# Performance work log

Hardware: AMD Instinct MI355X
Metric: run time of the kernel (lower is better)

## Reference

```python
import jax, jax.numpy as jnp
import numpy as np


def _gcn_conv(x, src, dst, W, b, n):
    # PyG GCNConv: linear -> add self-loops -> symmetric degree norm -> scatter-add -> bias
    h = x @ W  # [N, out]
    e = src.shape[0]
    loop = jnp.arange(n, dtype=src.dtype)
    s = jnp.concatenate([src, loop])
    d = jnp.concatenate([dst, loop])
    w = jnp.ones(e + n, dtype=x.dtype)
    deg = jax.ops.segment_sum(w, d, num_segments=n)              # in-degree incl. self-loop
    dinv = jnp.where(deg > 0, jax.lax.rsqrt(deg), 0.0)
    norm = dinv[s] * dinv[d]                                     # [E+N]
    out = jax.ops.segment_sum(h[s] * norm[:, None], d, num_segments=n)
    return out + b


def setup_inputs() -> dict:
    key = jax.random.key(0)
    ks = jax.random.split(key, 8)
    N, E = 100000, 1600000
    in_dim, hid, hid1, out_dim = 256, 128, 64, 40
    x = jax.random.normal(ks[0], (N, in_dim), dtype=jnp.float32)
    edge_index = jax.random.randint(ks[1], (2, E), 0, N, dtype=jnp.int32)
    W1 = jax.random.normal(ks[2], (in_dim, hid), dtype=jnp.float32) * (1.0 / np.sqrt(in_dim))
    b1 = jnp.zeros((hid,), jnp.float32)
    W2 = jax.random.normal(ks[3], (hid, hid1), dtype=jnp.float32) * (1.0 / np.sqrt(hid))
    b2 = jnp.zeros((hid1,), jnp.float32)
    Wo = jax.random.normal(ks[4], (hid1, out_dim), dtype=jnp.float32) * (1.0 / np.sqrt(hid1))
    bo = jnp.zeros((out_dim,), jnp.float32)
    return {"x": x, "edge_index": edge_index, "W1": W1, "b1": b1,
            "W2": W2, "b2": b2, "Wo": Wo, "bo": bo}


def reference(x, edge_index, W1, b1, W2, b2, Wo, bo):
    n = x.shape[0]
    src, dst = edge_index[0], edge_index[1]
    h = jax.nn.relu(_gcn_conv(x, src, dst, W1, b1, n))
    # F.dropout(training=False) is identity in inference
    h = _gcn_conv(h, src, dst, W2, b2, n)
    logits = h @ Wo + bo
    return jax.nn.log_softmax(logits, axis=1)
```

## Files before the change

### kernel.cpp

```cpp
#include <hip/hip_runtime.h>
#include <hip/hip_bf16.h>

typedef unsigned short u16;
typedef unsigned int u32;
typedef __attribute__((ext_vector_type(8))) short bf16x8;
typedef __attribute__((ext_vector_type(4))) float f32x4;
typedef __attribute__((ext_vector_type(4))) u16 u16x4;

__device__ __forceinline__ u16 f2bf(float f) {
    __hip_bfloat16 h = __float2bfloat16(f);
    return *reinterpret_cast<u16*>(&h);
}
__device__ __forceinline__ float bf_lo(u32 u) {
    union { u32 u; float f; } v; v.u = u << 16; return v.f;
}
__device__ __forceinline__ float bf_hi(u32 u) {
    union { u32 u; float f; } v; v.u = u & 0xFFFF0000u; return v.f;
}
__device__ __forceinline__ u32 pack2(float a, float b) {
    return (u32)f2bf(a) | ((u32)f2bf(b) << 16);
}

#define NB2 256
#define CHUNK 2048

__global__ void init_kernel(const float* __restrict__ W1, u16* __restrict__ B1, int K1, int N1,
                            const float* __restrict__ W2, u16* __restrict__ B2, int K2, int N2,
                            int* __restrict__ bcur, u32* __restrict__ g1pad,
                            u32* __restrict__ g2pad) {
    int i = blockIdx.x * 256 + threadIdx.x;
    int sz1 = K1 * N1;
    if (i < sz1) {
        int n = i / K1, k = i - n * K1;
        B1[i] = f2bf(W1[(size_t)k * N1 + n]);
    } else if (i - sz1 < K2 * N2) {
        int j = i - sz1;
        int n = j / K2, k = j - n * K2;
        B2[j] = f2bf(W2[(size_t)k * N2 + n]);
    }
    if (blockIdx.x == 0) {
        int t = threadIdx.x;
        bcur[t] = 0;
        if (t < 64) g1pad[t] = 0;
        if (t < 32) g2pad[t] = 0;
    }
}

__launch_bounds__(256)
__global__ void route(const int* __restrict__ src, const int* __restrict__ dst, int E, int R2,
                      int* __restrict__ bcur, int2* __restrict__ bp, int bcap) {
    __shared__ int cnt[NB2];
    __shared__ int cur[NB2];
    const int tid = threadIdx.x;
    const int base = blockIdx.x * CHUNK;
    cnt[tid] = 0;
    __syncthreads();
#pragma unroll
    for (int i = 0; i < CHUNK / 256; i++) {
        int e = base + i * 256 + tid;
        if (e < E) atomicAdd(&cnt[dst[e] / R2], 1);
    }
    __syncthreads();
    {
        int c = cnt[tid];
        cur[tid] = c ? atomicAdd(&bcur[tid], c) : 0;
    }
    __syncthreads();
#pragma unroll
    for (int i = 0; i < CHUNK / 256; i++) {
        int e = base + i * 256 + tid;
        if (e < E) {
            int d = dst[e], s = src[e];
            int b = d / R2;
            int pos = atomicAdd(&cur[b], 1);
            if (pos < bcap) bp[(size_t)b * bcap + pos] = (int2){s, d};
        }
    }
}

__launch_bounds__(256)
__global__ void build_csr(const int2* __restrict__ bp2, const int* __restrict__ bcnt2, int bcap2,
                          int sreg, int R2, int N,
                          int* __restrict__ rs, int* __restrict__ re,
                          float* __restrict__ dinv, int* __restrict__ srcids) {
    __shared__ int2 pl[8300];
    __shared__ int bins[400];
    __shared__ int tsum[256];
    const int b = blockIdx.x;
    const int tid = threadIdx.x;
    const int lo = b * R2;
    int hi = lo + R2; if (hi > N) hi = N;
    const int nb = hi - lo;
    if (nb <= 0) return;
    int cnt = bcnt2[b];
    if (cnt > bcap2) cnt = bcap2;
    const int2* mine = bp2 + (size_t)b * bcap2;

    for (int i = tid; i < nb; i += 256) bins[i] = 0;
    for (int i = tid; i < cnt; i += 256) pl[i] = mine[i];
    __syncthreads();
    for (int i = tid; i < cnt; i += 256) atomicAdd(&bins[pl[i].y - lo], 1);
    __syncthreads();

    const int base4 = tid * 4;
    int creal[4], cpad[4], ex[4];
    int run = 0;
#pragma unroll
    for (int k = 0; k < 4; k++) {
        int idx = base4 + k;
        creal[k] = 0; cpad[k] = 0; ex[k] = 0;
        if (idx < nb) {
            int c = bins[idx];
            creal[k] = c;
            cpad[k] = (c + 3) & ~3;
            dinv[lo + idx] = rsqrtf((float)c + 1.0f);
            ex[k] = run;
            run += cpad[k];
        }
    }
    tsum[tid] = run;
    __syncthreads();
    for (int off = 1; off < 256; off <<= 1) {
        int u = (tid >= off) ? tsum[tid - off] : 0;
        __syncthreads();
        tsum[tid] += u;
        __syncthreads();
    }
    const int toff = ((tid > 0) ? tsum[tid - 1] : 0) + b * sreg;
    __syncthreads();
#pragma unroll
    for (int k = 0; k < 4; k++) {
        int idx = base4 + k;
        if (idx < nb) {
            int st = toff + ex[k];
            bins[idx] = st;
            rs[lo + idx] = st;
            re[lo + idx] = st + cpad[k];
            for (int q = creal[k]; q < cpad[k]; q++) srcids[st + q] = N;
        }
    }
    __syncthreads();
    for (int i = tid; i < cnt; i += 256) {
        int2 p = pl[i];
        int pos = atomicAdd(&bins[p.y - lo], 1);
        srcids[pos] = p.x;
    }
}

template <int K, int BN, int IFR, int JFR, int WM, int WN, bool ABF16>
__launch_bounds__(256)
__global__ void gemm_mfma(const void* __restrict__ Av, const u16* __restrict__ Bt,
                          const float* __restrict__ dinv, u16* __restrict__ G, int M) {
    constexpr int BM = 128, BK = 32, BKP = 40;
    __shared__ u16 As[BM][BKP];
    __shared__ u16 Bs[BN][BKP];
    const int tid = threadIdx.x;
    const int lane = tid & 63, wave = tid >> 6;
    const int r = lane & 15, g = lane >> 4;
    const int wm = wave % WM, wn = wave / WM;
    const int m0 = blockIdx.x * BM;

    f32x4 acc[IFR][JFR];
#pragma unroll
    for (int i = 0; i < IFR; i++)
#pragma unroll
        for (int j = 0; j < JFR; j++) acc[i][j] = (f32x4){0.f, 0.f, 0.f, 0.f};

    for (int k0 = 0; k0 < K; k0 += BK) {
#pragma unroll
        for (int p = 0; p < 4; p++) {
            int q = tid + p * 256;
            int row = q >> 3, kq = (q & 7) << 2;
            int gr = m0 + row; if (gr >= M) gr = M - 1;
            if constexpr (ABF16) {
                const u16* A = (const u16*)Av;
                *(u16x4*)&As[row][kq] = *(const u16x4*)(A + (size_t)gr * K + k0 + kq);
            } else {
                const float* A = (const float*)Av;
                float4 a = *(const float4*)(A + (size_t)gr * K + k0 + kq);
                u16x4 v = { f2bf(a.x), f2bf(a.y), f2bf(a.z), f2bf(a.w) };
                *(u16x4*)&As[row][kq] = v;
            }
        }
#pragma unroll
        for (int p = 0; p < BN / 32; p++) {
            int q = tid + p * 256;
            int row = q >> 3, kq = (q & 7) << 2;
            *(u16x4*)&Bs[row][kq] = *(const u16x4*)(Bt + (size_t)row * K + k0 + kq);
        }
        __syncthreads();

        bf16x8 af[IFR], bfr[JFR];
#pragma unroll
        for (int i = 0; i < IFR; i++)
            af[i] = *(const bf16x8*)&As[wm * (IFR * 16) + i * 16 + r][g * 8];
#pragma unroll
        for (int j = 0; j < JFR; j++)
            bfr[j] = *(const bf16x8*)&Bs[wn * (JFR * 16) + j * 16 + r][g * 8];
#pragma unroll
        for (int i = 0; i < IFR; i++)
#pragma unroll
            for (int j = 0; j < JFR; j++)
                acc[i][j] = __builtin_amdgcn_mfma_f32_16x16x32_bf16(af[i], bfr[j], acc[i][j], 0, 0, 0);
        __syncthreads();
    }

#pragma unroll
    for (int i = 0; i < IFR; i++) {
#pragma unroll
        for (int t = 0; t < 4; t++) {
            int row = m0 + wm * (IFR * 16) + i * 16 + g * 4 + t;
            if (row < M) {
                float dn = dinv[row];
#pragma unroll
                for (int j = 0; j < JFR; j++) {
                    int col = wn * (JFR * 16) + j * 16 + r;
                    G[(size_t)row * BN + col] = f2bf(acc[i][j][t] * dn);
                }
            }
        }
    }
}

#define ACC8(v) { a0 += bf_lo(v.x); a1 += bf_hi(v.x); a2 += bf_lo(v.y); a3 += bf_hi(v.y); \
                  a4 += bf_lo(v.z); a5 += bf_hi(v.z); a6 += bf_lo(v.w); a7 += bf_hi(v.w); }

__launch_bounds__(256)
__global__ void agg128(const uint4* __restrict__ g1, const float4* __restrict__ bias,
                       const int* __restrict__ rs, const int* __restrict__ re,
                       const int* __restrict__ srcids, const float* __restrict__ dinv,
                       uint4* __restrict__ h1, int n) {
    const int tq = threadIdx.x >> 4;
    const int c  = threadIdx.x & 15;
    const int node = blockIdx.x * 16 + tq;
    if (node >= n) return;
    const float dn = dinv[node];
    uint4 sv = g1[(size_t)node * 16 + c];
    float a0 = bf_lo(sv.x), a1 = bf_hi(sv.x), a2 = bf_lo(sv.y), a3 = bf_hi(sv.y);
    float a4 = bf_lo(sv.z), a5 = bf_hi(sv.z), a6 = bf_lo(sv.w), a7 = bf_hi(sv.w);

    int j = rs[node] >> 2;
    const int jend = re[node] >> 2;
    const int4* ip = (const int4*)srcids;
    if (j < jend) {
        int4 idx = ip[j];
        for (++j; j < jend; ++j) {
            uint4 v0 = g1[(size_t)idx.x * 16 + c];
            uint4 v1 = g1[(size_t)idx.y * 16 + c];
            uint4 v2 = g1[(size_t)idx.z * 16 + c];
            uint4 v3 = g1[(size_t)idx.w * 16 + c];
            int4 nxt = ip[j];
            ACC8(v0); ACC8(v1); ACC8(v2); ACC8(v3);
            idx = nxt;
        }
        uint4 v0 = g1[(size_t)idx.x * 16 + c];
        uint4 v1 = g1[(size_t)idx.y * 16 + c];
        uint4 v2 = g1[(size_t)idx.z * 16 + c];
        uint4 v3 = g1[(size_t)idx.w * 16 + c];
        ACC8(v0); ACC8(v1); ACC8(v2); ACC8(v3);
    }

    float4 b0 = bias[c * 2], b1v = bias[c * 2 + 1];
    uint4 w;
    w.x = pack2(fmaxf(a0 * dn + b0.x, 0.f), fmaxf(a1 * dn + b0.y, 0.f));
    w.y = pack2(fmaxf(a2 * dn + b0.z, 0.f), fmaxf(a3 * dn + b0.w, 0.f));
    w.z = pack2(fmaxf(a4 * dn + b1v.x, 0.f), fmaxf(a5 * dn + b1v.y, 0.f));
    w.w = pack2(fmaxf(a6 * dn + b1v.z, 0.f), fmaxf(a7 * dn + b1v.w, 0.f));
    h1[(size_t)node * 16 + c] = w;
}

__launch_bounds__(256)
__global__ void agg64out(const uint2* __restrict__ g2, const float4* __restrict__ bias,
                         const int* __restrict__ rs, const int* __restrict__ re,
                         const int* __restrict__ srcids, const float* __restrict__ dinv,
                         const float* __restrict__ Wo, const float* __restrict__ bo,
                         float* __restrict__ out, int n) {
    __shared__ float Ws[64 * 40];
    __shared__ float bs[40];
    __shared__ float h2s[16][68];
    for (int i = threadIdx.x; i < 64 * 40; i += 256) Ws[i] = Wo[i];
    if (threadIdx.x < 40) bs[threadIdx.x] = bo[threadIdx.x];

    const int tq = threadIdx.x >> 4;
    const int c  = threadIdx.x & 15;
    const int node = blockIdx.x * 16 + tq;
    if (node < n) {
        const float dn = dinv[node];
        uint2 sv = g2[(size_t)node * 16 + c];
        float a0 = bf_lo(sv.x), a1 = bf_hi(sv.x), a2 = bf_lo(sv.y), a3 = bf_hi(sv.y);
        int j = rs[node] >> 2;
        const int jend = re[node] >> 2;
        const int4* ip = (const int4*)srcids;
        if (j < jend) {
            int4 idx = ip[j];
            for (++j; j < jend; ++j) {
                uint2 v0 = g2[(size_t)idx.x * 16 + c];
                uint2 v1 = g2[(size_t)idx.y * 16 + c];
                uint2 v2 = g2[(size_t)idx.z * 16 + c];
                uint2 v3 = g2[(size_t)idx.w * 16 + c];
                int4 nxt = ip[j];
                a0 += (bf_lo(v0.x) + bf_lo(v1.x)) + (bf_lo(v2.x) + bf_lo(v3.x));
                a1 += (bf_hi(v0.x) + bf_hi(v1.x)) + (bf_hi(v2.x) + bf_hi(v3.x));
                a2 += (bf_lo(v0.y) + bf_lo(v1.y)) + (bf_lo(v2.y) + bf_lo(v3.y));
                a3 += (bf_hi(v0.y) + bf_hi(v1.y)) + (bf_hi(v2.y) + bf_hi(v3.y));
                idx = nxt;
            }
            uint2 v0 = g2[(size_t)idx.x * 16 + c];
            uint2 v1 = g2[(size_t)idx.y * 16 + c];
            uint2 v2 = g2[(size_t)idx.z * 16 + c];
            uint2 v3 = g2[(size_t)idx.w * 16 + c];
            a0 += (bf_lo(v0.x) + bf_lo(v1.x)) + (bf_lo(v2.x) + bf_lo(v3.x));
            a1 += (bf_hi(v0.x) + bf_hi(v1.x)) + (bf_hi(v2.x) + bf_hi(v3.x));
            a2 += (bf_lo(v0.y) + bf_lo(v1.y)) + (bf_lo(v2.y) + bf_lo(v3.y));
            a3 += (bf_hi(v0.y) + bf_hi(v1.y)) + (bf_hi(v2.y) + bf_hi(v3.y));
        }
        float4 bb = bias[c];
        float4 hv = { a0 * dn + bb.x, a1 * dn + bb.y, a2 * dn + bb.z, a3 * dn + bb.w };
        *(float4*)&h2s[tq][c * 4] = hv;
    }
    __syncthreads();

    if (node < n) {
        const int j2 = (c < 8) ? (c + 32) : 39;
        float l0 = bs[c], l1 = bs[c + 16], l2 = bs[j2];
#pragma unroll 8
        for (int k = 0; k < 64; k++) {
            float hk = h2s[tq][k];
            l0 = fmaf(hk, Ws[k * 40 + c], l0);
            l1 = fmaf(hk, Ws[k * 40 + c + 16], l1);
            l2 = fmaf(hk, Ws[k * 40 + j2], l2);
        }
        float m = fmaxf(fmaxf(l0, l1), (c < 8) ? l2 : -3.0e38f);
#pragma unroll
        for (int o = 1; o < 16; o <<= 1) m = fmaxf(m, __shfl_xor(m, o));
        float s = expf(l0 - m) + expf(l1 - m) + ((c < 8) ? expf(l2 - m) : 0.f);
#pragma unroll
        for (int o = 1; o < 16; o <<= 1) s += __shfl_xor(s, o);
        float lse = m + logf(s);
        float* op = out + (size_t)node * 40;
        op[c] = l0 - lse;
        op[c + 16] = l1 - lse;
        if (c < 8) op[c + 32] = l2 - lse;
    }
}

extern "C" void kernel_launch(void* const* d_in, const int* in_sizes, int n_in,
                              void* d_out, int out_size, void* d_ws, size_t ws_size,
                              hipStream_t stream) {
    const float* x  = (const float*)d_in[0];
    const int*   ei = (const int*)d_in[1];
    const float* W1 = (const float*)d_in[2];
    const float* b1 = (const float*)d_in[3];
    const float* W2 = (const float*)d_in[4];
    const float* b2 = (const float*)d_in[5];
    const float* Wo = (const float*)d_in[6];
    const float* bo = (const float*)d_in[7];
    float* out = (float*)d_out;

    const int HID  = in_sizes[3];
    const int IN   = in_sizes[2] / HID;
    const int HID1 = in_sizes[5];
    const int N = in_sizes[0] / IN;
    const int E = in_sizes[1] / 2;
    const int* src = ei;
    const int* dst = ei + E;

    const int R2 = (N + NB2 - 1) / NB2;
    const int bcap2 = E / NB2 + 2048;
    const int sreg  = (bcap2 + 3 * R2 + 32 + 3) & ~3;

    char* ws = (char*)d_ws;
    size_t off = 0;
    auto alloc = [&](size_t bytes) -> void* {
        void* p = ws + off;
        off += (bytes + 255) / 256 * 256;
        return p;
    };
    float* dinv   = (float*)alloc((size_t)N * 4);
    int*   rs     = (int*)alloc((size_t)N * 4);
    int*   re     = (int*)alloc((size_t)N * 4);
    int*   bcur   = (int*)alloc(NB2 * 4);
    int*   srcids = (int*)alloc((size_t)NB2 * sreg * 4);
    u16*   W1t    = (u16*)alloc((size_t)IN * HID * 2);
    u16*   W2t    = (u16*)alloc((size_t)HID * HID1 * 2);
    size_t bp2Bytes = (size_t)NB2 * bcap2 * 8;
    size_t gBytes = (size_t)(N + 1) * HID * 2;
    size_t sharedBytes = (gBytes > bp2Bytes) ? gBytes : bp2Bytes;
    char*  shared = (char*)alloc(sharedBytes);
    int2*  bp2    = (int2*)shared;
    u16*   g1     = (u16*)shared;
    u16*   h1     = (u16*)alloc((size_t)N * HID * 2);
    u16*   g2     = (u16*)alloc((size_t)(N + 1) * HID1 * 2);

    init_kernel<<<(IN * HID + HID * HID1 + 255) / 256, 256, 0, stream>>>(
        W1, W1t, IN, HID, W2, W2t, HID, HID1,
        bcur, (u32*)g1 + (size_t)N * 64, (u32*)g2 + (size_t)N * 32);

    const int nchunk = (E + CHUNK - 1) / CHUNK;
    route<<<nchunk, 256, 0, stream>>>(src, dst, E, R2, bcur, bp2, bcap2);
    build_csr<<<NB2, 256, 0, stream>>>(bp2, bcur, bcap2, sreg, R2, N, rs, re, dinv, srcids);

    const int gblocks = (N + 127) / 128;
    gemm_mfma<256, 128, 4, 4, 2, 2, false><<<gblocks, 256, 0, stream>>>(x, W1t, dinv, g1, N);
    agg128<<<(N + 15) / 16, 256, 0, stream>>>((const uint4*)g1, (const float4*)b1,
                                              rs, re, srcids, dinv, (uint4*)h1, N);

    gemm_mfma<128, 64, 2, 4, 4, 1, true><<<gblocks, 256, 0, stream>>>(h1, W2t, dinv, g2, N);
    agg64out<<<(N + 15) / 16, 256, 0, stream>>>((const uint2*)g2, (const float4*)b2,
                                                rs, re, srcids, dinv, Wo, bo, out, N);

    (void)ws_size; (void)n_in; (void)out_size; (void)HID1;
}
```

Before: 203.3 us.

## Fuse edge routing with first GEMM and apply source normalization during aggregation

The edge-bucketing kernel and the first feature GEMM are merged into one launch whose blocks alternate between routing and GEMM work, so the two independent stages can overlap. Because the GEMM no longer waits for the degree computation, source-side dinv scaling moves out of the GEMM epilogue and into agg128, which loads dinv per neighbour and uses FMA. The bucket buffer and g1 no longer share memory, which raises the workspace footprint. A padded dinv entry is zeroed for the padding node. The cost is an extra per-edge dinv gather in the aggregation.

```diff
diff --git a/kernel.cpp b/kernel.cpp
--- a/kernel.cpp
+++ b/kernel.cpp
@@ -27,7 +27,7 @@
 __global__ void init_kernel(const float* __restrict__ W1, u16* __restrict__ B1, int K1, int N1,
                             const float* __restrict__ W2, u16* __restrict__ B2, int K2, int N2,
                             int* __restrict__ bcur, u32* __restrict__ g1pad,
-                            u32* __restrict__ g2pad) {
+                            u32* __restrict__ g2pad, float* __restrict__ dinv, int N) {
     int i = blockIdx.x * 256 + threadIdx.x;
     int sz1 = K1 * N1;
     if (i < sz1) {
@@ -43,16 +43,17 @@
         bcur[t] = 0;
         if (t < 64) g1pad[t] = 0;
         if (t < 32) g2pad[t] = 0;
-    }
-}
-
-__launch_bounds__(256)
-__global__ void route(const int* __restrict__ src, const int* __restrict__ dst, int E, int R2,
-                      int* __restrict__ bcur, int2* __restrict__ bp, int bcap) {
-    __shared__ int cnt[NB2];
-    __shared__ int cur[NB2];
+        if (t == 0) dinv[N] = 0.f;
+    }
+}
+
+__device__ void route_body(int bid, char* smem, const int* __restrict__ src,
+                           const int* __restrict__ dst, int E, int R2,
+                           int* __restrict__ bcur, int2* __restrict__ bp, int bcap) {
+    int* cnt = (int*)smem;
+    int* cur = cnt + NB2;
     const int tid = threadIdx.x;
-    const int base = blockIdx.x * CHUNK;
+    const int base = bid * CHUNK;
     cnt[tid] = 0;
     __syncthreads();
 #pragma unroll
@@ -75,6 +76,90 @@
             int pos = atomicAdd(&cur[b], 1);
             if (pos < bcap) bp[(size_t)b * bcap + pos] = (int2){s, d};
         }
+    }
+}
+
+__device__ void gemm1_body(int bid, char* smem, const float* __restrict__ A,
+                           const u16* __restrict__ Bt, u16* __restrict__ G, int M) {
+    constexpr int K = 256, BM = 128, BN = 128, BK = 32, BKP = 40, IFR = 4, JFR = 4, WM = 2;
+    u16 (*As)[BKP] = (u16(*)[BKP])smem;
+    u16 (*Bs)[BKP] = (u16(*)[BKP])(smem + BM * BKP * 2);
+    const int tid = threadIdx.x;
+    const int lane = tid & 63, wave = tid >> 6;
+    const int r = lane & 15, g = lane >> 4;
+    const int wm = wave % WM, wn = wave / WM;
+    const int m0 = bid * BM;
+
+    f32x4 acc[IFR][JFR];
+#pragma unroll
+    for (int i = 0; i < IFR; i++)
+#pragma unroll
+        for (int j = 0; j < JFR; j++) acc[i][j] = (f32x4){0.f, 0.f, 0.f, 0.f};
+
+    for (int k0 = 0; k0 < K; k0 += BK) {
+#pragma unroll
+        for (int p = 0; p < 4; p++) {
+            int q = tid + p * 256;
+            int row = q >> 3, kq = (q & 7) << 2;
+            int gr = m0 + row; if (gr >= M) gr = M - 1;
+            float4 a = *(const float4*)(A + (size_t)gr * K + k0 + kq);
+            u16x4 v = { f2bf(a.x), f2bf(a.y), f2bf(a.z), f2bf(a.w) };
+            *(u16x4*)&As[row][kq] = v;
+        }
+#pragma unroll
+        for (int p = 0; p < BN / 32; p++) {
+            int q = tid + p * 256;
+            int row = q >> 3, kq = (q & 7) << 2;
+            *(u16x4*)&Bs[row][kq] = *(const u16x4*)(Bt + (size_t)row * K + k0 + kq);
+        }
+        __syncthreads();
+
+        bf16x8 af[IFR], bfr[JFR];
+#pragma unroll
+        for (int i = 0; i < IFR; i++)
+            af[i] = *(const bf16x8*)&As[wm * (IFR * 16) + i * 16 + r][g * 8];
+#pragma unroll
+        for (int j = 0; j < JFR; j++)
+            bfr[j] = *(const bf16x8*)&Bs[wn * (JFR * 16) + j * 16 + r][g * 8];
+#pragma unroll
+        for (int i = 0; i < IFR; i++)
+#pragma unroll
+            for (int j = 0; j < JFR; j++)
+                acc[i][j] = __builtin_amdgcn_mfma_f32_16x16x32_bf16(af[i], bfr[j], acc[i][j], 0, 0, 0);
+        __syncthreads();
+    }
+
+#pragma unroll
+    for (int i = 0; i < IFR; i++) {
+#pragma unroll
+        for (int t = 0; t < 4; t++) {
+            int row = m0 + wm * (IFR * 16) + i * 16 + g * 4 + t;
+            if (row < M) {
+#pragma unroll
+                for (int j = 0; j < JFR; j++) {
+                    int col = wn * (JFR * 16) + j * 16 + r;
+                    G[(size_t)row * BN + col] = f2bf(acc[i][j][t]);
+                }
+            }
+        }
+    }
+}
+
+__launch_bounds__(256)
+__global__ void route_gemm1(const int* __restrict__ src, const int* __restrict__ dst, int E, int R2,
+                            int* __restrict__ bcur, int2* __restrict__ bp, int bcap, int nroute,
+                            const float* __restrict__ x, const u16* __restrict__ W1t,
+                            u16* __restrict__ g1, int M, int ngemm) {
+    __shared__ alignas(16) char smem[20480];
+    int bid = blockIdx.x;
+    int g = (nroute < ngemm) ? nroute : ngemm;
+    if (bid < 2 * g) {
+        if (bid & 1) route_body(bid >> 1, smem, src, dst, E, R2, bcur, bp, bcap);
+        else         gemm1_body(bid >> 1, smem, x, W1t, g1, M);
+    } else {
+        int rm = bid - 2 * g;
+        if (ngemm > nroute) gemm1_body(g + rm, smem, x, W1t, g1, M);
+        else                route_body(g + rm, smem, src, dst, E, R2, bcur, bp, bcap);
     }
 }
 
@@ -147,9 +232,9 @@
     }
 }
 
-template <int K, int BN, int IFR, int JFR, int WM, int WN, bool ABF16>
+template <int K, int BN, int IFR, int JFR, int WM, int WN>
 __launch_bounds__(256)
-__global__ void gemm_mfma(const void* __restrict__ Av, const u16* __restrict__ Bt,
+__global__ void gemm_mfma(const u16* __restrict__ A, const u16* __restrict__ Bt,
                           const float* __restrict__ dinv, u16* __restrict__ G, int M) {
     constexpr int BM = 128, BK = 32, BKP = 40;
     __shared__ u16 As[BM][BKP];
@@ -172,15 +257,7 @@
             int q = tid + p * 256;
             int row = q >> 3, kq = (q & 7) << 2;
             int gr = m0 + row; if (gr >= M) gr = M - 1;
-            if constexpr (ABF16) {
-                const u16* A = (const u16*)Av;
-                *(u16x4*)&As[row][kq] = *(const u16x4*)(A + (size_t)gr * K + k0 + kq);
-            } else {
-                const float* A = (const float*)Av;
-                float4 a = *(const float4*)(A + (size_t)gr * K + k0 + kq);
-                u16x4 v = { f2bf(a.x), f2bf(a.y), f2bf(a.z), f2bf(a.w) };
-                *(u16x4*)&As[row][kq] = v;
-            }
+            *(u16x4*)&As[row][kq] = *(const u16x4*)(A + (size_t)gr * K + k0 + kq);
         }
 #pragma unroll
         for (int p = 0; p < BN / 32; p++) {
@@ -222,8 +299,10 @@
     }
 }
 
-#define ACC8(v) { a0 += bf_lo(v.x); a1 += bf_hi(v.x); a2 += bf_lo(v.y); a3 += bf_hi(v.y); \
-                  a4 += bf_lo(v.z); a5 += bf_hi(v.z); a6 += bf_lo(v.w); a7 += bf_hi(v.w); }
+#define ACCW(v, wt) { a0 = fmaf(bf_lo(v.x), wt, a0); a1 = fmaf(bf_hi(v.x), wt, a1); \
+                      a2 = fmaf(bf_lo(v.y), wt, a2); a3 = fmaf(bf_hi(v.y), wt, a3); \
+                      a4 = fmaf(bf_lo(v.z), wt, a4); a5 = fmaf(bf_hi(v.z), wt, a5); \
+                      a6 = fmaf(bf_lo(v.w), wt, a6); a7 = fmaf(bf_hi(v.w), wt, a7); }
 
 __launch_bounds__(256)
 __global__ void agg128(const uint4* __restrict__ g1, const float4* __restrict__ bias,
@@ -236,8 +315,8 @@
     if (node >= n) return;
     const float dn = dinv[node];
     uint4 sv = g1[(size_t)node * 16 + c];
-    float a0 = bf_lo(sv.x), a1 = bf_hi(sv.x), a2 = bf_lo(sv.y), a3 = bf_hi(sv.y);
-    float a4 = bf_lo(sv.z), a5 = bf_hi(sv.z), a6 = bf_lo(sv.w), a7 = bf_hi(sv.w);
+    float a0 = bf_lo(sv.x) * dn, a1 = bf_hi(sv.x) * dn, a2 = bf_lo(sv.y) * dn, a3 = bf_hi(sv.y) * dn;
+    float a4 = bf_lo(sv.z) * dn, a5 = bf_hi(sv.z) * dn, a6 = bf_lo(sv.w) * dn, a7 = bf_hi(sv.w) * dn;
 
     int j = rs[node] >> 2;
     const int jend = re[node] >> 2;
@@ -245,19 +324,21 @@
     if (j < jend) {
         int4 idx = ip[j];
         for (++j; j < jend; ++j) {
+            float w0 = dinv[idx.x], w1 = dinv[idx.y], w2 = dinv[idx.z], w3 = dinv[idx.w];
             uint4 v0 = g1[(size_t)idx.x * 16 + c];
             uint4 v1 = g1[(size_t)idx.y * 16 + c];
             uint4 v2 = g1[(size_t)idx.z * 16 + c];
             uint4 v3 = g1[(size_t)idx.w * 16 + c];
             int4 nxt = ip[j];
-            ACC8(v0); ACC8(v1); ACC8(v2); ACC8(v3);
+            ACCW(v0, w0); ACCW(v1, w1); ACCW(v2, w2); ACCW(v3, w3);
             idx = nxt;
         }
+        float w0 = dinv[idx.x], w1 = dinv[idx.y], w2 = dinv[idx.z], w3 = dinv[idx.w];
         uint4 v0 = g1[(size_t)idx.x * 16 + c];
         uint4 v1 = g1[(size_t)idx.y * 16 + c];
         uint4 v2 = g1[(size_t)idx.z * 16 + c];
         uint4 v3 = g1[(size_t)idx.w * 16 + c];
-        ACC8(v0); ACC8(v1); ACC8(v2); ACC8(v3);
+        ACCW(v0, w0); ACCW(v1, w1); ACCW(v2, w2); ACCW(v3, w3);
     }
 
     float4 b0 = bias[c * 2], b1v = bias[c * 2 + 1];
@@ -376,36 +457,33 @@
         off += (bytes + 255) / 256 * 256;
         return p;
     };
-    float* dinv   = (float*)alloc((size_t)N * 4);
+    float* dinv   = (float*)alloc((size_t)(N + 1) * 4);
     int*   rs     = (int*)alloc((size_t)N * 4);
     int*   re     = (int*)alloc((size_t)N * 4);
     int*   bcur   = (int*)alloc(NB2 * 4);
     int*   srcids = (int*)alloc((size_t)NB2 * sreg * 4);
     u16*   W1t    = (u16*)alloc((size_t)IN * HID * 2);
     u16*   W2t    = (u16*)alloc((size_t)HID * HID1 * 2);
-    size_t bp2Bytes = (size_t)NB2 * bcap2 * 8;
-    size_t gBytes = (size_t)(N + 1) * HID * 2;
-    size_t sharedBytes = (gBytes > bp2Bytes) ? gBytes : bp2Bytes;
-    char*  shared = (char*)alloc(sharedBytes);
-    int2*  bp2    = (int2*)shared;
-    u16*   g1     = (u16*)shared;
+    int2*  bp2    = (int2*)alloc((size_t)NB2 * bcap2 * 8);
+    u16*   g1     = (u16*)alloc((size_t)(N + 1) * HID * 2);
     u16*   h1     = (u16*)alloc((size_t)N * HID * 2);
     u16*   g2     = (u16*)alloc((size_t)(N + 1) * HID1 * 2);
 
     init_kernel<<<(IN * HID + HID * HID1 + 255) / 256, 256, 0, stream>>>(
         W1, W1t, IN, HID, W2, W2t, HID, HID1,
-        bcur, (u32*)g1 + (size_t)N * 64, (u32*)g2 + (size_t)N * 32);
-
-    const int nchunk = (E + CHUNK - 1) / CHUNK;
-    route<<<nchunk, 256, 0, stream>>>(src, dst, E, R2, bcur, bp2, bcap2);
+        bcur, (u32*)g1 + (size_t)N * 64, (u32*)g2 + (size_t)N * 32, dinv, N);
+
+    const int nroute = (E + CHUNK - 1) / CHUNK;
+    const int ngemm  = (N + 127) / 128;
+    route_gemm1<<<nroute + ngemm, 256, 0, stream>>>(
+        src, dst, E, R2, bcur, bp2, bcap2, nroute, x, W1t, g1, N, ngemm);
+
     build_csr<<<NB2, 256, 0, stream>>>(bp2, bcur, bcap2, sreg, R2, N, rs, re, dinv, srcids);
 
-    const int gblocks = (N + 127) / 128;
-    gemm_mfma<256, 128, 4, 4, 2, 2, false><<<gblocks, 256, 0, stream>>>(x, W1t, dinv, g1, N);
     agg128<<<(N + 15) / 16, 256, 0, stream>>>((const uint4*)g1, (const float4*)b1,
                                               rs, re, srcids, dinv, (uint4*)h1, N);
 
-    gemm_mfma<128, 64, 2, 4, 4, 1, true><<<gblocks, 256, 0, stream>>>(h1, W2t, dinv, g2, N);
+    gemm_mfma<128, 64, 2, 4, 4, 1><<<ngemm, 256, 0, stream>>>(h1, W2t, dinv, g2, N);
     agg64out<<<(N + 15) / 16, 256, 0, stream>>>((const uint2*)g2, (const float4*)b2,
                                                 rs, re, srcids, dinv, Wo, bo, out, N);
 
```

Result: slower. 215.6 us (+6.0%).
